# Kernel tuning notes

Measured on AMD Instinct MI355X. Metric: run time of the kernel, lower is better.

The kernel has to match this reference:

```python
import jax, jax.numpy as jnp
import numpy as np

N = 50000      # nodes
E = 800000     # edges (avg degree 16)
F_IN = 128
HID = 64
NCLS = 40
K = 2          # num_stacks
T = 2          # num_layers (shared weights)


def setup_inputs() -> dict:
    key = jax.random.key(0)
    ks = jax.random.split(key, 10)
    s = 0.05
    return {
        "x": jax.random.normal(ks[0], (N, F_IN), dtype=jnp.float32),
        "edge_index": jax.random.randint(ks[1], (2, E), 0, N),
        "w1_init": jax.random.normal(ks[2], (K, F_IN, HID), dtype=jnp.float32) * s,
        "w1": jax.random.normal(ks[3], (K, HID, HID), dtype=jnp.float32) * s,
        "v1": jax.random.normal(ks[4], (K, F_IN, HID), dtype=jnp.float32) * s,
        "b1": jax.random.normal(ks[5], (K, HID), dtype=jnp.float32) * s,
        "w2_init": jax.random.normal(ks[6], (K, HID, NCLS), dtype=jnp.float32) * s,
        "w2": jax.random.normal(ks[7], (K, NCLS, NCLS), dtype=jnp.float32) * s,
        "v2": jax.random.normal(ks[8], (K, HID, NCLS), dtype=jnp.float32) * s,
        "b2": jax.random.normal(ks[9], (K, NCLS), dtype=jnp.float32) * s,
    }


def _gcn_norm(src, dst, n):
    # PyG gcn_norm with add_self_loops=False: deg over destination, sym norm
    deg = jax.ops.segment_sum(jnp.ones_like(dst, dtype=jnp.float32), dst, num_segments=n)
    dinv = jnp.where(deg > 0, 1.0 / jnp.sqrt(deg), 0.0)
    return dinv[src] * dinv[dst]  # [E]


def _arma_conv(x, src, dst, norm, n, w_init, w, v, b, act):
    # x: [N, Fin]; w_init: [K, Fin, Fout]; w: [K, Fout, Fout]; v: [K, Fin, Fout]; b: [K, Fout]
    root = jnp.einsum('nf,kfg->kng', x, v)  # [K, N, Fout], dropout=0 -> identity
    out = None
    for t in range(T):
        if t == 0:
            h = jnp.einsum('nf,kfg->kng', x, w_init)
        else:
            h = jnp.einsum('knf,kfg->kng', out, w)
        # sparse neighbor aggregation: out[i] = sum_{(j->i)} norm_e * h[j]
        agg = jax.vmap(
            lambda hk: jax.ops.segment_sum(hk[src] * norm[:, None], dst, num_segments=n)
        )(h)  # [K, N, Fout]
        out = act(agg + root + b[:, None, :])
    return out.mean(axis=0)  # mean over stacks -> [N, Fout]


def reference(x, edge_index, w1_init, w1, v1, b1, w2_init, w2, v2, b2):
    src, dst = edge_index[0], edge_index[1]
    norm = _gcn_norm(src, dst, N)
    h = _arma_conv(x, src, dst, norm, N, w1_init, w1, v1, b1, jax.nn.relu)
    h = jax.nn.relu(h)  # wrapper ReLU; dropout is identity in eval
    o = _arma_conv(h, src, dst, norm, N, w2_init, w2, v2, b2, lambda z: z)
    return jax.nn.log_softmax(o, axis=1)
```

## Files before the change

kernel.cpp:

```cpp
#include <hip/hip_runtime.h>
#include <hip/hip_bf16.h>
#include <math.h>

#define N_NODES 50000
#define F_IN 128
#define HID 64
#define NCLS 40
#define K_STACKS 2
#define SCAN_TILE 1024
#define NBLK_CNT 256

typedef __attribute__((ext_vector_type(8))) short short8;
typedef __attribute__((ext_vector_type(4))) float floatx4;
typedef __attribute__((ext_vector_type(2))) float floatx2;

__device__ __forceinline__ unsigned int f32_to_bf16_bits(float f) {
    unsigned int u = __float_as_uint(f);
    return (u + 0x7fffu + ((u >> 16) & 1u)) >> 16;
}
__device__ __forceinline__ unsigned int pack_bf16x2(float a, float b) {
    return f32_to_bf16_bits(a) | (f32_to_bf16_bits(b) << 16);
}
__device__ __forceinline__ unsigned char f32_to_fp8(float v) {
    int pk = __builtin_amdgcn_cvt_pk_fp8_f32(v, v, 0, false);
    return (unsigned char)(pk & 0xff);
}


__global__ __launch_bounds__(256) void count_kernel(const int* __restrict__ dst,
                                                    int* __restrict__ counts,
                                                    int* __restrict__ tileSums, int E) {
    __shared__ int hist[256];
    __shared__ int ts[64];
    int blk = blockIdx.x, t = threadIdx.x;
    hist[t] = 0;
    if (t < 64) ts[t] = 0;
    __syncthreads();
    int chunk = (E + NBLK_CNT - 1) / NBLK_CNT;
    int s = blk * chunk, e = min(E, s + chunk);
    for (int i = s + t; i < e; i += 256) atomicAdd(&hist[dst[i] >> 8], 1);
    __syncthreads();
    counts[t * NBLK_CNT + blk] = hist[t];
    atomicAdd(&ts[t >> 2], hist[t]);
    __syncthreads();
    if (t < 64) atomicAdd(&tileSums[t], ts[t]);
}

__global__ __launch_bounds__(256) void scan_phase3_excl(const int* __restrict__ in,
                                                        const int* __restrict__ tileSums,
                                                        int* __restrict__ out, int n) {
    __shared__ int lds[256];
    __shared__ int tsum[64];
    int b = blockIdx.x, t = threadIdx.x;
    if (t < 64) tsum[t] = tileSums[t];
    int base = b * SCAN_TILE + t * 4;
    int e[4];
    int s = 0;
#pragma unroll
    for (int i = 0; i < 4; ++i) {
        e[i] = (base + i < n) ? in[base + i] : 0;
        s += e[i];
    }
    lds[t] = s;
    __syncthreads();
    int v = s;
    for (int off = 1; off < 256; off <<= 1) {
        int add = (t >= off) ? lds[t - off] : 0;
        __syncthreads();
        v += add;
        lds[t] = v;
        __syncthreads();
    }
    int toff = 0;
    for (int i = 0; i < b; ++i) toff += tsum[i];
    int run = (t == 0 ? 0 : lds[t - 1]) + toff;
#pragma unroll
    for (int i = 0; i < 4; ++i) {
        if (base + i < n) {
            out[base + i] = run;
            run += e[i];
        }
    }
}

__global__ __launch_bounds__(256) void bucket_scatter_kernel(const int* __restrict__ src,
                                                             const int* __restrict__ dst,
                                                             const int* __restrict__ scanned,
                                                             unsigned int* __restrict__ pairs,
                                                             int E) {
    __shared__ int cur[256];
    int blk = blockIdx.x, t = threadIdx.x;
    cur[t] = scanned[t * NBLK_CNT + blk];
    __syncthreads();
    int chunk = (E + NBLK_CNT - 1) / NBLK_CNT;
    int s0 = blk * chunk, e0 = min(E, s0 + chunk);
    for (int i = s0 + t; i < e0; i += 256) {
        int d = dst[i];
        int pos = atomicAdd(&cur[d >> 8], 1);
        pairs[pos] = (unsigned int)src[i] | ((unsigned int)(d & 255) << 16);
    }
}

__global__ __launch_bounds__(256) void csr_build_kernel(const unsigned int* __restrict__ pairs,
                                                        const int* __restrict__ scanned,
                                                        int* __restrict__ row_ptr,
                                                        float* __restrict__ dinv,
                                                        int* __restrict__ col, int N, int E) {
    __shared__ int degl[256], lds[256], curl[256], sb[2];
    int b = blockIdx.x, t = threadIdx.x;
    if (t == 0) {
        sb[0] = scanned[b * NBLK_CNT];
        sb[1] = (b + 1 < 256) ? scanned[(b + 1) * NBLK_CNT] : E;
    }
    degl[t] = 0;
    __syncthreads();
    int bstart = sb[0], bend = sb[1];
    for (int e = bstart + t; e < bend; e += 256) {
        atomicAdd(&degl[(pairs[e] >> 16) & 255], 1);
    }
    __syncthreads();
    int d = degl[t];
    lds[t] = d;
    __syncthreads();
    int v = d;
    for (int off = 1; off < 256; off <<= 1) {
        int add = (t >= off) ? lds[t - off] : 0;
        __syncthreads();
        v += add;
        lds[t] = v;
        __syncthreads();
    }
    int excl = v - d;
    int node = b * 256 + t;
    if (node <= N) row_ptr[node] = bstart + excl;
    if (node < N) dinv[node] = (d > 0) ? (1.0f / sqrtf((float)d)) : 0.0f;
    curl[t] = excl;
    __syncthreads();
    for (int e = bstart + t; e < bend; e += 256) {
        unsigned int p = pairs[e];
        int ln = (p >> 16) & 255;
        int pos = atomicAdd(&curl[ln], 1);
        col[bstart + pos] = (int)(p & 0xffffu);
    }
}

__device__ __forceinline__ void wt_one(const float* __restrict__ in,
                                       unsigned short* __restrict__ out, int li, int C, int F,
                                       int CP) {
    int k = li / (F * CP);
    int r = li - k * F * CP;
    int f = r / CP;
    int c = r - f * CP;
    out[li] = (c < C) ? (unsigned short)f32_to_bf16_bits(in[((size_t)k * C + c) * F + f]) : 0;
}

__global__ void wt_all_kernel(const float* v1, const float* w1i, const float* w1,
                              const float* v2, const float* w2i, const float* w2,
                              unsigned short* v1t, unsigned short* w1it, unsigned short* w1t,
                              unsigned short* v2t, unsigned short* w2it, unsigned short* w2t) {
    int i = blockIdx.x * blockDim.x + threadIdx.x;
    if (i < 16384) wt_one(v1, v1t, i, 128, 64, 128);
    else if (i < 32768) wt_one(w1i, w1it, i - 16384, 128, 64, 128);
    else if (i < 40960) wt_one(w1, w1t, i - 32768, 64, 64, 64);
    else if (i < 46080) wt_one(v2, v2t, i - 40960, 64, 40, 64);
    else if (i < 51200) wt_one(w2i, w2it, i - 46080, 64, 40, 64);
    else if (i < 56320) wt_one(w2, w2t, i - 51200, 40, 40, 64);
}

template <int CINP>
__device__ __forceinline__ void stage_A(const void* A, unsigned short* At, size_t abase,
                                        int n0, int t, int N, int CREAL, int a_bf16) {
    constexpr int CP8 = CINP / 8;
    constexpr int MS = CP8 - 1;
    constexpr int SH = (CP8 == 16) ? 4 : 3;
    for (int i = t; i < 64 * CP8; i += 256) {
        int n = i >> SH;
        int c = i & MS;
        uint4 w = make_uint4(0u, 0u, 0u, 0u);
        int gn = n0 + n;
        if (gn < N && c * 8 < CREAL) {
            if (a_bf16) {
                w = *(const uint4*)((const unsigned short*)A + abase + (size_t)gn * CREAL + c * 8);
            } else {
                const float* srcp = (const float*)A + abase + (size_t)gn * CREAL + c * 8;
                float4 f0 = *(const float4*)(srcp);
                float4 f1 = *(const float4*)(srcp + 4);
                w.x = pack_bf16x2(f0.x, f0.y);
                w.y = pack_bf16x2(f0.z, f0.w);
                w.z = pack_bf16x2(f1.x, f1.y);
                w.w = pack_bf16x2(f1.z, f1.w);
            }
        }
        *(uint4*)(At + n * CINP + ((c ^ (n & MS)) << 3)) = w;
    }
}

template <int CINP>
__device__ __forceinline__ void stage_B(const unsigned short* Bk, unsigned short* Bs, int t,
                                        int COUT) {
    constexpr int CP8 = CINP / 8;
    constexpr int MS = CP8 - 1;
    constexpr int SH = (CP8 == 16) ? 4 : 3;
    for (int i = t; i < COUT * CP8; i += 256) {
        int f = i >> SH;
        int c = i & MS;
        uint4 w = *(const uint4*)(Bk + f * CINP + c * 8);
        *(uint4*)(Bs + f * CINP + ((c ^ (f & MS)) << 3)) = w;
    }
}

template <int CINP>
__global__ __launch_bounds__(256) void gemm_mfma(
    const void* __restrict__ A, const unsigned short* __restrict__ Bt,
    void* __restrict__ out, const float* __restrict__ scale, int N, int COUT, int CREAL,
    int a_per_k, int a_bf16, int out_fp8, int do_scale, int out_inter) {
    constexpr int MS = CINP / 8 - 1;
    __shared__ __align__(16) unsigned short At[64 * CINP];
    __shared__ __align__(16) unsigned short Bs[64 * CINP];

    const int k = blockIdx.y;
    const int n0 = blockIdx.x * 64;
    const int t = threadIdx.x;
    stage_A<CINP>(A, At, a_per_k ? (size_t)k * N * CREAL : (size_t)0, n0, t, N, CREAL, a_bf16);
    stage_B<CINP>(Bt + (size_t)k * COUT * CINP, Bs, t, COUT);
    __syncthreads();

    const int lane = t & 63;
    const int wv = t >> 6;
    const int quad = lane >> 4;
    const int li = lane & 15;
    const int m0 = wv * 16;

    floatx4 acc[4] = {{0.f, 0.f, 0.f, 0.f}, {0.f, 0.f, 0.f, 0.f},
                      {0.f, 0.f, 0.f, 0.f}, {0.f, 0.f, 0.f, 0.f}};
    const int am = (m0 + li) & MS;
#pragma unroll
    for (int kc = 0; kc < CINP / 32; ++kc) {
        int cc = kc * 4 + quad;
        short8 a = *(const short8*)(At + (m0 + li) * CINP + ((cc ^ am) << 3));
#pragma unroll
        for (int nt = 0; nt < 4; ++nt) {
            if (nt * 16 < COUT) {
                int f = nt * 16 + li;
                short8 b = *(const short8*)(Bs + f * CINP + ((cc ^ (f & MS)) << 3));
                acc[nt] = __builtin_amdgcn_mfma_f32_16x16x32_bf16(a, b, acc[nt], 0, 0, 0);
            }
        }
    }

    float sc[4] = {1.f, 1.f, 1.f, 1.f};
    if (do_scale) {
#pragma unroll
        for (int r = 0; r < 4; ++r) {
            int node = n0 + m0 + quad * 4 + r;
            sc[r] = (node < N) ? scale[node] : 1.f;
        }
    }
#pragma unroll
    for (int nt = 0; nt < 4; ++nt) {
        if (nt * 16 >= COUT) continue;
        int f = nt * 16 + li;
        if (f >= COUT) continue;
#pragma unroll
        for (int r = 0; r < 4; ++r) {
            int node = n0 + m0 + quad * 4 + r;
            if (node < N) {
                float val = acc[nt][r] * sc[r];
                if (out_inter) {
                    size_t o = (size_t)node * 2 * COUT + (size_t)k * COUT + f;
                    if (out_fp8)
                        ((unsigned char*)out)[o] = f32_to_fp8(val);
                    else
                        ((unsigned short*)out)[o] = (unsigned short)f32_to_bf16_bits(val);
                } else {
                    size_t o = ((size_t)k * N + node) * COUT + f;
                    ((float*)out)[o] = val;
                }
            }
        }
    }
}

template <int CINP>
__global__ __launch_bounds__(256) void gemm2_mfma(
    const void* __restrict__ A, const unsigned short* __restrict__ Bt1,
    const unsigned short* __restrict__ Bt2, unsigned short* __restrict__ out1,
    unsigned char* __restrict__ out2, const float* __restrict__ scale, int N, int COUT,
    int CREAL, int a_bf16) {
    constexpr int MS = CINP / 8 - 1;
    __shared__ __align__(16) unsigned short At[64 * CINP];
    __shared__ __align__(16) unsigned short Bs1[64 * CINP];
    __shared__ __align__(16) unsigned short Bs2[64 * CINP];

    const int n0 = blockIdx.x * 64;
    const int t = threadIdx.x;
    stage_A<CINP>(A, At, (size_t)0, n0, t, N, CREAL, a_bf16);

    const int lane = t & 63;
    const int wv = t >> 6;
    const int quad = lane >> 4;
    const int li = lane & 15;
    const int m0 = wv * 16;
    const int am = (m0 + li) & MS;

    float sc[4];
#pragma unroll
    for (int r = 0; r < 4; ++r) {
        int node = n0 + m0 + quad * 4 + r;
        sc[r] = (node < N) ? scale[node] : 1.f;
    }

    for (int k = 0; k < 2; ++k) {
        if (k) __syncthreads();
        stage_B<CINP>(Bt1 + (size_t)k * COUT * CINP, Bs1, t, COUT);
        stage_B<CINP>(Bt2 + (size_t)k * COUT * CINP, Bs2, t, COUT);
        __syncthreads();

        floatx4 acc1[4] = {{0.f, 0.f, 0.f, 0.f}, {0.f, 0.f, 0.f, 0.f},
                           {0.f, 0.f, 0.f, 0.f}, {0.f, 0.f, 0.f, 0.f}};
        floatx4 acc2[4] = {{0.f, 0.f, 0.f, 0.f}, {0.f, 0.f, 0.f, 0.f},
                           {0.f, 0.f, 0.f, 0.f}, {0.f, 0.f, 0.f, 0.f}};
#pragma unroll
        for (int kc = 0; kc < CINP / 32; ++kc) {
            int cc = kc * 4 + quad;
            short8 a = *(const short8*)(At + (m0 + li) * CINP + ((cc ^ am) << 3));
#pragma unroll
            for (int nt = 0; nt < 4; ++nt) {
                if (nt * 16 < COUT) {
                    int f = nt * 16 + li;
                    int bo = f * CINP + ((cc ^ (f & MS)) << 3);
                    short8 b1 = *(const short8*)(Bs1 + bo);
                    short8 b2 = *(const short8*)(Bs2 + bo);
                    acc1[nt] = __builtin_amdgcn_mfma_f32_16x16x32_bf16(a, b1, acc1[nt], 0, 0, 0);
                    acc2[nt] = __builtin_amdgcn_mfma_f32_16x16x32_bf16(a, b2, acc2[nt], 0, 0, 0);
                }
            }
        }
#pragma unroll
        for (int nt = 0; nt < 4; ++nt) {
            if (nt * 16 >= COUT) continue;
            int f = nt * 16 + li;
            if (f >= COUT) continue;
#pragma unroll
            for (int r = 0; r < 4; ++r) {
                int node = n0 + m0 + quad * 4 + r;
                if (node < N) {
                    out1[((size_t)k * N + node) * COUT + f] =
                        (unsigned short)f32_to_bf16_bits(acc1[nt][r]);
                    out2[(size_t)node * 2 * COUT + (size_t)k * COUT + f] =
                        f32_to_fp8(acc2[nt][r] * sc[r]);
                }
            }
        }
    }
}

template <int F>
__global__ __launch_bounds__(256) void agg_kernel(
    const unsigned char* __restrict__ h8, const int* __restrict__ row_ptr,
    const int* __restrict__ col, const float* __restrict__ dinv,
    const unsigned short* __restrict__ rootb, const float* __restrict__ bias,
    void* __restrict__ out, int N, int do_relu, int mode) {
    constexpr int FH = F / 8;
    constexpr int ROWB = 2 * F;
    int wid = (blockIdx.x * blockDim.x + threadIdx.x) >> 6;
    int lane = threadIdx.x & 63;
    int half = lane >> 5;
    int l32 = lane & 31;
    int node = wid * 2 + half;
    bool valid = node < N;
    int e0 = 0, deg = 0;
    float dv = 0.f;
    if (valid) {
        e0 = row_ptr[node];
        deg = row_ptr[node + 1] - e0;
        dv = dinv[node];
    }
    const int sub = l32 >> 4;
    const int fq = l32 & 15;
    const int kk = fq >> 3;
    const int fqq = fq & 7;
    const int fqc = (fqq < FH) ? fqq : (FH - 1);
    const int foff = kk * F + fqc * 8;

    float acc[8] = {};
    for (int w0 = 0; w0 < deg; w0 += 32) {
        int mye = w0 + l32;
        int c = (mye < deg) ? col[e0 + mye] : 0;
        int nch = min(deg - w0, 32);
        for (int base = 0; base < nch; base += 16) {
            uint2 v[8];
            float wj[8];
#pragma unroll
            for (int u = 0; u < 8; ++u) {
                int j = base + u * 2 + sub;
                int cj = __shfl(c, (half << 5) | (j & 31));
                bool ok = (j < nch);
                wj[u] = ok ? 1.f : 0.f;
                int cs = ok ? cj : 0;
                v[u] = *(const uint2*)(h8 + (size_t)cs * ROWB + foff);
            }
#pragma unroll
            for (int u = 0; u < 8; ++u) {
                floatx2 f0 = __builtin_amdgcn_cvt_pk_f32_fp8(v[u].x, false);
                floatx2 f1 = __builtin_amdgcn_cvt_pk_f32_fp8(v[u].x, true);
                floatx2 f2 = __builtin_amdgcn_cvt_pk_f32_fp8(v[u].y, false);
                floatx2 f3 = __builtin_amdgcn_cvt_pk_f32_fp8(v[u].y, true);
                acc[0] += wj[u] * f0.x;
                acc[1] += wj[u] * f0.y;
                acc[2] += wj[u] * f1.x;
                acc[3] += wj[u] * f1.y;
                acc[4] += wj[u] * f2.x;
                acc[5] += wj[u] * f2.y;
                acc[6] += wj[u] * f3.x;
                acc[7] += wj[u] * f3.y;
            }
        }
    }
#pragma unroll
    for (int i = 0; i < 8; ++i) acc[i] += __shfl_xor(acc[i], 16);

    size_t oc = ((size_t)kk * N + (valid ? node : 0)) * F + fqc * 8;
    uint4 rv = *(const uint4*)(rootb + oc);
    const float* bp = bias + kk * F + fqc * 8;
    float4 b0 = *(const float4*)(bp);
    float4 b1 = *(const float4*)(bp + 4);
    const unsigned int ru[4] = {rv.x, rv.y, rv.z, rv.w};
    float res[8];
#pragma unroll
    for (int q = 0; q < 4; ++q) {
        float rlo = __uint_as_float(ru[q] << 16);
        float rhi = __uint_as_float(ru[q] & 0xffff0000u);
        float blo = (q < 2) ? ((q == 0) ? b0.x : b0.z) : ((q == 2) ? b1.x : b1.z);
        float bhi = (q < 2) ? ((q == 0) ? b0.y : b0.w) : ((q == 2) ? b1.y : b1.w);
        res[2 * q] = acc[2 * q] * dv + rlo + blo;
        res[2 * q + 1] = acc[2 * q + 1] * dv + rhi + bhi;
    }
    if (do_relu) {
#pragma unroll
        for (int i = 0; i < 8; ++i) res[i] = fmaxf(res[i], 0.f);
    }
    if (mode == 0) {
        if (sub == 0 && fqq < FH && valid) {
            size_t o = ((size_t)kk * N + node) * F + fqq * 8;
            uint4 w;
            w.x = pack_bf16x2(res[0], res[1]);
            w.y = pack_bf16x2(res[2], res[3]);
            w.z = pack_bf16x2(res[4], res[5]);
            w.w = pack_bf16x2(res[6], res[7]);
            *(uint4*)((unsigned short*)out + o) = w;
        }
    } else {
        float mres[8];
#pragma unroll
        for (int i = 0; i < 8; ++i) mres[i] = 0.5f * (res[i] + __shfl_xor(res[i], 8));
        if (mode == 1) {
            if (sub == 0 && kk == 0 && fqq < FH && valid) {
                size_t o = (size_t)node * F + fqq * 8;
                *(float4*)((float*)out + o) = make_float4(mres[0], mres[1], mres[2], mres[3]);
                *(float4*)((float*)out + o + 4) = make_float4(mres[4], mres[5], mres[6], mres[7]);
            }
        } else {
            bool act = (fqq < FH);
            float lm = -INFINITY;
            if (act) {
#pragma unroll
                for (int i = 0; i < 8; ++i) lm = fmaxf(lm, mres[i]);
            }
#pragma unroll
            for (int m = 1; m < 8; m <<= 1) lm = fmaxf(lm, __shfl_xor(lm, m));
            float ls = 0.f;
            if (act) {
#pragma unroll
                for (int i = 0; i < 8; ++i) ls += expf(mres[i] - lm);
            }
#pragma unroll
            for (int m = 1; m < 8; m <<= 1) ls += __shfl_xor(ls, m);
            float lg = lm + logf(ls);
            if (sub == 0 && kk == 0 && act && valid) {
                size_t o = (size_t)node * F + fqq * 8;
                *(float4*)((float*)out + o) =
                    make_float4(mres[0] - lg, mres[1] - lg, mres[2] - lg, mres[3] - lg);
                *(float4*)((float*)out + o + 4) =
                    make_float4(mres[4] - lg, mres[5] - lg, mres[6] - lg, mres[7] - lg);
            }
        }
    }
}


static inline size_t align256(size_t x) { return (x + 255) & ~(size_t)255; }

extern "C" void kernel_launch(void* const* d_in, const int* in_sizes, int n_in,
                              void* d_out, int out_size, void* d_ws, size_t ws_size,
                              hipStream_t stream) {
    const float* x = (const float*)d_in[0];
    const int* ei = (const int*)d_in[1];
    const float* w1_init = (const float*)d_in[2];
    const float* w1 = (const float*)d_in[3];
    const float* v1 = (const float*)d_in[4];
    const float* b1 = (const float*)d_in[5];
    const float* w2_init = (const float*)d_in[6];
    const float* w2 = (const float*)d_in[7];
    const float* v2 = (const float*)d_in[8];
    const float* b2 = (const float*)d_in[9];

    const int N = in_sizes[0] / F_IN;
    const int E = in_sizes[1] / 2;
    const int* src = ei;
    const int* dst = ei + E;

    char* p = (char*)d_ws;
    auto take = [&](size_t bytes) {
        char* r = p;
        p += align256(bytes);
        return r;
    };
    float* dinv = (float*)take((size_t)N * 4);
    int* row_ptr = (int*)take((size_t)(N + 1) * 4);
    int* tileSums = (int*)take(256 * 4);
    int* counts = (int*)take((size_t)256 * NBLK_CNT * 4);
    int* scanned = (int*)take((size_t)256 * NBLK_CNT * 4);
    unsigned int* pairs = (unsigned int*)take((size_t)E * 4);
    int* col = (int*)take((size_t)E * 4);
    unsigned short* v1t = (unsigned short*)take((size_t)2 * 64 * 128 * 2);
    unsigned short* w1it = (unsigned short*)take((size_t)2 * 64 * 128 * 2);
    unsigned short* w1t = (unsigned short*)take((size_t)2 * 64 * 64 * 2);
    unsigned short* v2t = (unsigned short*)take((size_t)2 * 40 * 64 * 2);
    unsigned short* w2it = (unsigned short*)take((size_t)2 * 40 * 64 * 2);
    unsigned short* w2t = (unsigned short*)take((size_t)2 * 40 * 64 * 2);
    unsigned short* rootb = (unsigned short*)take((size_t)K_STACKS * N * HID * 2);
    unsigned char* hb8 = (unsigned char*)take((size_t)K_STACKS * N * HID);
    unsigned short* hc = (unsigned short*)take((size_t)K_STACKS * N * HID * 2);
    float* h1 = (float*)take((size_t)N * HID * 4);

    const int TB = 256;
    const int nCnt = 256 * NBLK_CNT;
    const int nScanBlocks = nCnt / SCAN_TILE;
    const int nBuckets = (N + 255) / 256;
    const int ntiles = (N + 63) / 64;

    hipMemsetAsync(tileSums, 0, 256, stream);
    count_kernel<<<NBLK_CNT, 256, 0, stream>>>(dst, counts, tileSums, E);
    scan_phase3_excl<<<nScanBlocks, 256, 0, stream>>>(counts, tileSums, scanned, nCnt);
    bucket_scatter_kernel<<<NBLK_CNT, 256, 0, stream>>>(src, dst, scanned, pairs, E);
    csr_build_kernel<<<nBuckets, 256, 0, stream>>>(pairs, scanned, row_ptr, dinv, col, N, E);

    wt_all_kernel<<<(56320 + TB - 1) / TB, TB, 0, stream>>>(v1, w1_init, w1, v2, w2_init, w2,
                                                            v1t, w1it, w1t, v2t, w2it, w2t);

    dim3 ggrid(ntiles, K_STACKS);
    const int agg_blocks = ((N + 1) / 2 + 3) / 4;

    gemm2_mfma<128><<<ntiles, 256, 0, stream>>>(x, v1t, w1it, rootb, hb8, dinv, N, HID, 128, 0);
    agg_kernel<HID><<<agg_blocks, 256, 0, stream>>>(hb8, row_ptr, col, dinv, rootb, b1, hc, N, 1, 0);
    gemm_mfma<64><<<ggrid, 256, 0, stream>>>(hc, w1t, hb8, dinv, N, HID, 64, 1, 1, 1, 1, 1);
    agg_kernel<HID><<<agg_blocks, 256, 0, stream>>>(hb8, row_ptr, col, dinv, rootb, b1, h1, N, 1, 1);

    gemm2_mfma<64><<<ntiles, 256, 0, stream>>>(h1, v2t, w2it, rootb, hb8, dinv, N, NCLS, 64, 0);
    agg_kernel<NCLS><<<agg_blocks, 256, 0, stream>>>(hb8, row_ptr, col, dinv, rootb, b2, hc, N, 0, 0);
    gemm_mfma<64><<<ggrid, 256, 0, stream>>>(hc, w2t, hb8, dinv, N, NCLS, 40, 1, 1, 1, 1, 1);
    agg_kernel<NCLS><<<agg_blocks, 256, 0, stream>>>(hb8, row_ptr, col, dinv, rootb, b2,
                                                     (float*)d_out, N, 0, 2);
}
```

Measured before the change: 288.0 us.

## Fuse aggregation with next-layer GEMM and merge weight prep into count kernel

Fuses the first sparse aggregation of each ARMA layer with the following per-stack GEMM in a single kernel. Aggregated rows go through LDS as bf16 and are fed straight into MFMA, so the intermediate bf16 buffer is never written to or read back from global memory. It also splits gemm2 across stacks via a remapped grid, folds weight transposition into the count kernel, and has the scan compute prefix offsets directly instead of using tileSums and a memset. In exchange the fused kernel has 64 nodes per block with serialized gathers, which may lower occupancy and parallelism in the aggregation phase.

```diff
diff --git a/kernel.cpp b/kernel.cpp
--- a/kernel.cpp
+++ b/kernel.cpp
@@ -9,6 +9,7 @@
 #define K_STACKS 2
 #define SCAN_TILE 1024
 #define NBLK_CNT 256
+#define WT_BLOCKS 220
 
 typedef __attribute__((ext_vector_type(8))) short short8;
 typedef __attribute__((ext_vector_type(4))) float floatx4;
@@ -26,33 +27,55 @@
     return (unsigned char)(pk & 0xff);
 }
 
-
-__global__ __launch_bounds__(256) void count_kernel(const int* __restrict__ dst,
-                                                    int* __restrict__ counts,
-                                                    int* __restrict__ tileSums, int E) {
+__device__ __forceinline__ void wt_one(const float* __restrict__ in,
+                                       unsigned short* __restrict__ out, int li, int C, int F,
+                                       int CP) {
+    int k = li / (F * CP);
+    int r = li - k * F * CP;
+    int f = r / CP;
+    int c = r - f * CP;
+    out[li] = (c < C) ? (unsigned short)f32_to_bf16_bits(in[((size_t)k * C + c) * F + f]) : 0;
+}
+
+__global__ __launch_bounds__(256) void count_wt_kernel(
+    const int* __restrict__ dst, int* __restrict__ counts, int E,
+    const float* v1, const float* w1i, const float* w1,
+    const float* v2, const float* w2i, const float* w2,
+    unsigned short* v1t, unsigned short* w1it, unsigned short* w1t,
+    unsigned short* v2t, unsigned short* w2it, unsigned short* w2t) {
+    int blk = blockIdx.x, t = threadIdx.x;
+    if (blk >= NBLK_CNT) {
+        int i = (blk - NBLK_CNT) * 256 + t;
+        if (i < 16384) wt_one(v1, v1t, i, 128, 64, 128);
+        else if (i < 32768) wt_one(w1i, w1it, i - 16384, 128, 64, 128);
+        else if (i < 40960) wt_one(w1, w1t, i - 32768, 64, 64, 64);
+        else if (i < 46080) wt_one(v2, v2t, i - 40960, 64, 40, 64);
+        else if (i < 51200) wt_one(w2i, w2it, i - 46080, 64, 40, 64);
+        else if (i < 56320) wt_one(w2, w2t, i - 51200, 40, 40, 64);
+        return;
+    }
     __shared__ int hist[256];
-    __shared__ int ts[64];
-    int blk = blockIdx.x, t = threadIdx.x;
     hist[t] = 0;
-    if (t < 64) ts[t] = 0;
     __syncthreads();
     int chunk = (E + NBLK_CNT - 1) / NBLK_CNT;
     int s = blk * chunk, e = min(E, s + chunk);
     for (int i = s + t; i < e; i += 256) atomicAdd(&hist[dst[i] >> 8], 1);
     __syncthreads();
     counts[t * NBLK_CNT + blk] = hist[t];
-    atomicAdd(&ts[t >> 2], hist[t]);
-    __syncthreads();
-    if (t < 64) atomicAdd(&tileSums[t], ts[t]);
 }
 
 __global__ __launch_bounds__(256) void scan_phase3_excl(const int* __restrict__ in,
-                                                        const int* __restrict__ tileSums,
                                                         int* __restrict__ out, int n) {
+    __shared__ int red[256];
     __shared__ int lds[256];
-    __shared__ int tsum[64];
     int b = blockIdx.x, t = threadIdx.x;
-    if (t < 64) tsum[t] = tileSums[t];
+    int part = 0;
+    int lim = b * SCAN_TILE;
+    for (int i = t * 4; i < lim; i += 1024) {
+        int4 v = *(const int4*)(in + i);
+        part += v.x + v.y + v.z + v.w;
+    }
+    red[t] = part;
     int base = b * SCAN_TILE + t * 4;
     int e[4];
     int s = 0;
@@ -63,6 +86,11 @@
     }
     lds[t] = s;
     __syncthreads();
+    for (int off = 128; off; off >>= 1) {
+        if (t < off) red[t] += red[t + off];
+        __syncthreads();
+    }
+    int toff = red[0];
     int v = s;
     for (int off = 1; off < 256; off <<= 1) {
         int add = (t >= off) ? lds[t - off] : 0;
@@ -71,8 +99,6 @@
         lds[t] = v;
         __syncthreads();
     }
-    int toff = 0;
-    for (int i = 0; i < b; ++i) toff += tsum[i];
     int run = (t == 0 ? 0 : lds[t - 1]) + toff;
 #pragma unroll
     for (int i = 0; i < 4; ++i) {
@@ -142,29 +168,6 @@
         int pos = atomicAdd(&curl[ln], 1);
         col[bstart + pos] = (int)(p & 0xffffu);
     }
-}
-
-__device__ __forceinline__ void wt_one(const float* __restrict__ in,
-                                       unsigned short* __restrict__ out, int li, int C, int F,
-                                       int CP) {
-    int k = li / (F * CP);
-    int r = li - k * F * CP;
-    int f = r / CP;
-    int c = r - f * CP;
-    out[li] = (c < C) ? (unsigned short)f32_to_bf16_bits(in[((size_t)k * C + c) * F + f]) : 0;
-}
-
-__global__ void wt_all_kernel(const float* v1, const float* w1i, const float* w1,
-                              const float* v2, const float* w2i, const float* w2,
-                              unsigned short* v1t, unsigned short* w1it, unsigned short* w1t,
-                              unsigned short* v2t, unsigned short* w2it, unsigned short* w2t) {
-    int i = blockIdx.x * blockDim.x + threadIdx.x;
-    if (i < 16384) wt_one(v1, v1t, i, 128, 64, 128);
-    else if (i < 32768) wt_one(w1i, w1it, i - 16384, 128, 64, 128);
-    else if (i < 40960) wt_one(w1, w1t, i - 32768, 64, 64, 64);
-    else if (i < 46080) wt_one(v2, v2t, i - 40960, 64, 40, 64);
-    else if (i < 51200) wt_one(w2i, w2it, i - 46080, 64, 40, 64);
-    else if (i < 56320) wt_one(w2, w2t, i - 51200, 40, 40, 64);
 }
 
 template <int CINP>
@@ -210,78 +213,6 @@
 }
 
 template <int CINP>
-__global__ __launch_bounds__(256) void gemm_mfma(
-    const void* __restrict__ A, const unsigned short* __restrict__ Bt,
-    void* __restrict__ out, const float* __restrict__ scale, int N, int COUT, int CREAL,
-    int a_per_k, int a_bf16, int out_fp8, int do_scale, int out_inter) {
-    constexpr int MS = CINP / 8 - 1;
-    __shared__ __align__(16) unsigned short At[64 * CINP];
-    __shared__ __align__(16) unsigned short Bs[64 * CINP];
-
-    const int k = blockIdx.y;
-    const int n0 = blockIdx.x * 64;
-    const int t = threadIdx.x;
-    stage_A<CINP>(A, At, a_per_k ? (size_t)k * N * CREAL : (size_t)0, n0, t, N, CREAL, a_bf16);
-    stage_B<CINP>(Bt + (size_t)k * COUT * CINP, Bs, t, COUT);
-    __syncthreads();
-
-    const int lane = t & 63;
-    const int wv = t >> 6;
-    const int quad = lane >> 4;
-    const int li = lane & 15;
-    const int m0 = wv * 16;
-
-    floatx4 acc[4] = {{0.f, 0.f, 0.f, 0.f}, {0.f, 0.f, 0.f, 0.f},
-                      {0.f, 0.f, 0.f, 0.f}, {0.f, 0.f, 0.f, 0.f}};
-    const int am = (m0 + li) & MS;
-#pragma unroll
-    for (int kc = 0; kc < CINP / 32; ++kc) {
-        int cc = kc * 4 + quad;
-        short8 a = *(const short8*)(At + (m0 + li) * CINP + ((cc ^ am) << 3));
-#pragma unroll
-        for (int nt = 0; nt < 4; ++nt) {
-            if (nt * 16 < COUT) {
-                int f = nt * 16 + li;
-                short8 b = *(const short8*)(Bs + f * CINP + ((cc ^ (f & MS)) << 3));
-                acc[nt] = __builtin_amdgcn_mfma_f32_16x16x32_bf16(a, b, acc[nt], 0, 0, 0);
-            }
-        }
-    }
-
-    float sc[4] = {1.f, 1.f, 1.f, 1.f};
-    if (do_scale) {
-#pragma unroll
-        for (int r = 0; r < 4; ++r) {
-            int node = n0 + m0 + quad * 4 + r;
-            sc[r] = (node < N) ? scale[node] : 1.f;
-        }
-    }
-#pragma unroll
-    for (int nt = 0; nt < 4; ++nt) {
-        if (nt * 16 >= COUT) continue;
-        int f = nt * 16 + li;
-        if (f >= COUT) continue;
-#pragma unroll
-        for (int r = 0; r < 4; ++r) {
-            int node = n0 + m0 + quad * 4 + r;
-            if (node < N) {
-                float val = acc[nt][r] * sc[r];
-                if (out_inter) {
-                    size_t o = (size_t)node * 2 * COUT + (size_t)k * COUT + f;
-                    if (out_fp8)
-                        ((unsigned char*)out)[o] = f32_to_fp8(val);
-                    else
-                        ((unsigned short*)out)[o] = (unsigned short)f32_to_bf16_bits(val);
-                } else {
-                    size_t o = ((size_t)k * N + node) * COUT + f;
-                    ((float*)out)[o] = val;
-                }
-            }
-        }
-    }
-}
-
-template <int CINP>
 __global__ __launch_bounds__(256) void gemm2_mfma(
     const void* __restrict__ A, const unsigned short* __restrict__ Bt1,
     const unsigned short* __restrict__ Bt2, unsigned short* __restrict__ out1,
@@ -292,16 +223,45 @@
     __shared__ __align__(16) unsigned short Bs1[64 * CINP];
     __shared__ __align__(16) unsigned short Bs2[64 * CINP];
 
-    const int n0 = blockIdx.x * 64;
+    const int id = blockIdx.x;
+    const int p = ((id >> 4) << 3) | (id & 7);
+    const int k = (id >> 3) & 1;
+    const int ntiles = (N + 63) >> 6;
+    if (p >= ntiles) return;
+    const int n0 = p * 64;
     const int t = threadIdx.x;
     stage_A<CINP>(A, At, (size_t)0, n0, t, N, CREAL, a_bf16);
+    stage_B<CINP>(Bt1 + (size_t)k * COUT * CINP, Bs1, t, COUT);
+    stage_B<CINP>(Bt2 + (size_t)k * COUT * CINP, Bs2, t, COUT);
+    __syncthreads();
 
     const int lane = t & 63;
     const int wv = t >> 6;
     const int quad = lane >> 4;
     const int li = lane & 15;
     const int m0 = wv * 16;
+
+    floatx4 acc1[4] = {{0.f, 0.f, 0.f, 0.f}, {0.f, 0.f, 0.f, 0.f},
+                       {0.f, 0.f, 0.f, 0.f}, {0.f, 0.f, 0.f, 0.f}};
+    floatx4 acc2[4] = {{0.f, 0.f, 0.f, 0.f}, {0.f, 0.f, 0.f, 0.f},
+                       {0.f, 0.f, 0.f, 0.f}, {0.f, 0.f, 0.f, 0.f}};
     const int am = (m0 + li) & MS;
+#pragma unroll
+    for (int kc = 0; kc < CINP / 32; ++kc) {
+        int cc = kc * 4 + quad;
+        short8 a = *(const short8*)(At + (m0 + li) * CINP + ((cc ^ am) << 3));
+#pragma unroll
+        for (int nt = 0; nt < 4; ++nt) {
+            if (nt * 16 < COUT) {
+                int f = nt * 16 + li;
+                int bo = f * CINP + ((cc ^ (f & MS)) << 3);
+                short8 b1 = *(const short8*)(Bs1 + bo);
+                short8 b2 = *(const short8*)(Bs2 + bo);
+                acc1[nt] = __builtin_amdgcn_mfma_f32_16x16x32_bf16(a, b1, acc1[nt], 0, 0, 0);
+                acc2[nt] = __builtin_amdgcn_mfma_f32_16x16x32_bf16(a, b2, acc2[nt], 0, 0, 0);
+            }
+        }
+    }
 
     float sc[4];
 #pragma unroll
@@ -309,30 +269,160 @@
         int node = n0 + m0 + quad * 4 + r;
         sc[r] = (node < N) ? scale[node] : 1.f;
     }
-
+#pragma unroll
+    for (int nt = 0; nt < 4; ++nt) {
+        if (nt * 16 >= COUT) continue;
+        int f = nt * 16 + li;
+        if (f >= COUT) continue;
+#pragma unroll
+        for (int r = 0; r < 4; ++r) {
+            int node = n0 + m0 + quad * 4 + r;
+            if (node < N) {
+                out1[((size_t)k * N + node) * COUT + f] =
+                    (unsigned short)f32_to_bf16_bits(acc1[nt][r]);
+                out2[(size_t)node * 2 * COUT + (size_t)k * COUT + f] =
+                    f32_to_fp8(acc2[nt][r] * sc[r]);
+            }
+        }
+    }
+}
+
+template <int F, int CINP>
+__global__ __launch_bounds__(256) void agg_gemm_kernel(
+    const unsigned char* __restrict__ h8, const int* __restrict__ row_ptr,
+    const int* __restrict__ col, const float* __restrict__ dinv,
+    const unsigned short* __restrict__ rootb, const float* __restrict__ bias,
+    const unsigned short* __restrict__ Bt, unsigned char* __restrict__ out2,
+    int N, int do_relu) {
+    constexpr int FH = F / 8;
+    constexpr int ROWB = 2 * F;
+    constexpr int COUT = F;
+    constexpr int MS = CINP / 8 - 1;
+    __shared__ __align__(16) unsigned short At[2][64 * CINP];
+    __shared__ __align__(16) unsigned short Bs[2][64 * CINP];
+
+    const int n0 = blockIdx.x * 64;
+    const int t = threadIdx.x;
+
+    for (int i = t; i < 2 * 64 * (CINP / 8); i += 256)
+        ((uint4*)At)[i] = make_uint4(0u, 0u, 0u, 0u);
+    stage_B<CINP>(Bt, Bs[0], t, COUT);
+    stage_B<CINP>(Bt + (size_t)COUT * CINP, Bs[1], t, COUT);
+    __syncthreads();
+
+    const int lane = t & 63;
+    const int wv = t >> 6;
+    const int half = lane >> 5;
+    const int l32 = lane & 31;
+    const int sub = l32 >> 4;
+    const int fq = l32 & 15;
+    const int kk = fq >> 3;
+    const int fqq = fq & 7;
+    const int fqc = (fqq < FH) ? fqq : (FH - 1);
+    const int foff = kk * F + fqc * 8;
+
+    for (int r = 0; r < 8; ++r) {
+        int ln = r * 8 + wv * 2 + half;
+        int node = n0 + ln;
+        bool valid = node < N;
+        int e0 = 0, deg = 0;
+        float dv = 0.f;
+        if (valid) {
+            e0 = row_ptr[node];
+            deg = row_ptr[node + 1] - e0;
+            dv = dinv[node];
+        }
+        float acc[8] = {};
+        for (int w0 = 0; w0 < deg; w0 += 32) {
+            int mye = w0 + l32;
+            int c = (mye < deg) ? col[e0 + mye] : 0;
+            int nch = min(deg - w0, 32);
+            for (int base = 0; base < nch; base += 16) {
+                uint2 v[8];
+                float wj[8];
+#pragma unroll
+                for (int u = 0; u < 8; ++u) {
+                    int j = base + u * 2 + sub;
+                    int cj = __shfl(c, (half << 5) | (j & 31));
+                    bool ok = (j < nch);
+                    wj[u] = ok ? 1.f : 0.f;
+                    int cs = ok ? cj : 0;
+                    v[u] = *(const uint2*)(h8 + (size_t)cs * ROWB + foff);
+                }
+#pragma unroll
+                for (int u = 0; u < 8; ++u) {
+                    floatx2 f0 = __builtin_amdgcn_cvt_pk_f32_fp8(v[u].x, false);
+                    floatx2 f1 = __builtin_amdgcn_cvt_pk_f32_fp8(v[u].x, true);
+                    floatx2 f2 = __builtin_amdgcn_cvt_pk_f32_fp8(v[u].y, false);
+                    floatx2 f3 = __builtin_amdgcn_cvt_pk_f32_fp8(v[u].y, true);
+                    acc[0] += wj[u] * f0.x;
+                    acc[1] += wj[u] * f0.y;
+                    acc[2] += wj[u] * f1.x;
+                    acc[3] += wj[u] * f1.y;
+                    acc[4] += wj[u] * f2.x;
+                    acc[5] += wj[u] * f2.y;
+                    acc[6] += wj[u] * f3.x;
+                    acc[7] += wj[u] * f3.y;
+                }
+            }
+        }
+#pragma unroll
+        for (int i = 0; i < 8; ++i) acc[i] += __shfl_xor(acc[i], 16);
+
+        size_t oc = ((size_t)kk * N + (valid ? node : 0)) * F + fqc * 8;
+        uint4 rv = *(const uint4*)(rootb + oc);
+        const float* bp = bias + kk * F + fqc * 8;
+        float4 b0 = *(const float4*)(bp);
+        float4 b1 = *(const float4*)(bp + 4);
+        const unsigned int ru[4] = {rv.x, rv.y, rv.z, rv.w};
+        float res[8];
+#pragma unroll
+        for (int q = 0; q < 4; ++q) {
+            float rlo = __uint_as_float(ru[q] << 16);
+            float rhi = __uint_as_float(ru[q] & 0xffff0000u);
+            float blo = (q < 2) ? ((q == 0) ? b0.x : b0.z) : ((q == 2) ? b1.x : b1.z);
+            float bhi = (q < 2) ? ((q == 0) ? b0.y : b0.w) : ((q == 2) ? b1.y : b1.w);
+            res[2 * q] = acc[2 * q] * dv + rlo + blo;
+            res[2 * q + 1] = acc[2 * q + 1] * dv + rhi + bhi;
+        }
+        if (do_relu) {
+#pragma unroll
+            for (int i = 0; i < 8; ++i) res[i] = fmaxf(res[i], 0.f);
+        }
+        if (sub == 0 && fqq < FH && valid) {
+            uint4 w;
+            w.x = pack_bf16x2(res[0], res[1]);
+            w.y = pack_bf16x2(res[2], res[3]);
+            w.z = pack_bf16x2(res[4], res[5]);
+            w.w = pack_bf16x2(res[6], res[7]);
+            *(uint4*)(&At[kk][ln * CINP + ((fqq ^ (ln & MS)) << 3)]) = w;
+        }
+    }
+    __syncthreads();
+
+    const int quad = lane >> 4;
+    const int li = lane & 15;
+    const int m0 = wv * 16;
+    const int am = (m0 + li) & MS;
+    float sc[4];
+#pragma unroll
+    for (int r = 0; r < 4; ++r) {
+        int node = n0 + m0 + quad * 4 + r;
+        sc[r] = (node < N) ? dinv[node] : 1.f;
+    }
     for (int k = 0; k < 2; ++k) {
-        if (k) __syncthreads();
-        stage_B<CINP>(Bt1 + (size_t)k * COUT * CINP, Bs1, t, COUT);
-        stage_B<CINP>(Bt2 + (size_t)k * COUT * CINP, Bs2, t, COUT);
-        __syncthreads();
-
-        floatx4 acc1[4] = {{0.f, 0.f, 0.f, 0.f}, {0.f, 0.f, 0.f, 0.f},
-                           {0.f, 0.f, 0.f, 0.f}, {0.f, 0.f, 0.f, 0.f}};
-        floatx4 acc2[4] = {{0.f, 0.f, 0.f, 0.f}, {0.f, 0.f, 0.f, 0.f},
-                           {0.f, 0.f, 0.f, 0.f}, {0.f, 0.f, 0.f, 0.f}};
+        floatx4 acc[4] = {{0.f, 0.f, 0.f, 0.f}, {0.f, 0.f, 0.f, 0.f},
+                          {0.f, 0.f, 0.f, 0.f}, {0.f, 0.f, 0.f, 0.f}};
 #pragma unroll
         for (int kc = 0; kc < CINP / 32; ++kc) {
             int cc = kc * 4 + quad;
-            short8 a = *(const short8*)(At + (m0 + li) * CINP + ((cc ^ am) << 3));
+            short8 a = *(const short8*)(&At[k][(m0 + li) * CINP + ((cc ^ am) << 3)]);
 #pragma unroll
             for (int nt = 0; nt < 4; ++nt) {
                 if (nt * 16 < COUT) {
                     int f = nt * 16 + li;
-                    int bo = f * CINP + ((cc ^ (f & MS)) << 3);
-                    short8 b1 = *(const short8*)(Bs1 + bo);
-                    short8 b2 = *(const short8*)(Bs2 + bo);
-                    acc1[nt] = __builtin_amdgcn_mfma_f32_16x16x32_bf16(a, b1, acc1[nt], 0, 0, 0);
-                    acc2[nt] = __builtin_amdgcn_mfma_f32_16x16x32_bf16(a, b2, acc2[nt], 0, 0, 0);
+                    short8 b = *(const short8*)(&Bs[k][f * CINP + ((cc ^ (f & MS)) << 3)]);
+                    acc[nt] = __builtin_amdgcn_mfma_f32_16x16x32_bf16(a, b, acc[nt], 0, 0, 0);
                 }
             }
         }
@@ -344,12 +434,9 @@
 #pragma unroll
             for (int r = 0; r < 4; ++r) {
                 int node = n0 + m0 + quad * 4 + r;
-                if (node < N) {
-                    out1[((size_t)k * N + node) * COUT + f] =
-                        (unsigned short)f32_to_bf16_bits(acc1[nt][r]);
+                if (node < N)
                     out2[(size_t)node * 2 * COUT + (size_t)k * COUT + f] =
-                        f32_to_fp8(acc2[nt][r] * sc[r]);
-                }
+                        f32_to_fp8(acc[nt][r] * sc[r]);
             }
         }
     }
@@ -440,50 +527,38 @@
 #pragma unroll
         for (int i = 0; i < 8; ++i) res[i] = fmaxf(res[i], 0.f);
     }
-    if (mode == 0) {
-        if (sub == 0 && fqq < FH && valid) {
-            size_t o = ((size_t)kk * N + node) * F + fqq * 8;
-            uint4 w;
-            w.x = pack_bf16x2(res[0], res[1]);
-            w.y = pack_bf16x2(res[2], res[3]);
-            w.z = pack_bf16x2(res[4], res[5]);
-            w.w = pack_bf16x2(res[6], res[7]);
-            *(uint4*)((unsigned short*)out + o) = w;
+    float mres[8];
+#pragma unroll
+    for (int i = 0; i < 8; ++i) mres[i] = 0.5f * (res[i] + __shfl_xor(res[i], 8));
+    if (mode == 1) {
+        if (sub == 0 && kk == 0 && fqq < FH && valid) {
+            size_t o = (size_t)node * F + fqq * 8;
+            *(float4*)((float*)out + o) = make_float4(mres[0], mres[1], mres[2], mres[3]);
+            *(float4*)((float*)out + o + 4) = make_float4(mres[4], mres[5], mres[6], mres[7]);
         }
     } else {
-        float mres[8];
-#pragma unroll
-        for (int i = 0; i < 8; ++i) mres[i] = 0.5f * (res[i] + __shfl_xor(res[i], 8));
-        if (mode == 1) {
-            if (sub == 0 && kk == 0 && fqq < FH && valid) {
-                size_t o = (size_t)node * F + fqq * 8;
-                *(float4*)((float*)out + o) = make_float4(mres[0], mres[1], mres[2], mres[3]);
-                *(float4*)((float*)out + o + 4) = make_float4(mres[4], mres[5], mres[6], mres[7]);
-            }
-        } else {
-            bool act = (fqq < FH);
-            float lm = -INFINITY;
-            if (act) {
-#pragma unroll
-                for (int i = 0; i < 8; ++i) lm = fmaxf(lm, mres[i]);
-            }
-#pragma unroll
-            for (int m = 1; m < 8; m <<= 1) lm = fmaxf(lm, __shfl_xor(lm, m));
-            float ls = 0.f;
-            if (act) {
-#pragma unroll
-                for (int i = 0; i < 8; ++i) ls += expf(mres[i] - lm);
-            }
-#pragma unroll
-            for (int m = 1; m < 8; m <<= 1) ls += __shfl_xor(ls, m);
-            float lg = lm + logf(ls);
-            if (sub == 0 && kk == 0 && act && valid) {
-                size_t o = (size_t)node * F + fqq * 8;
-                *(float4*)((float*)out + o) =
-                    make_float4(mres[0] - lg, mres[1] - lg, mres[2] - lg, mres[3] - lg);
-                *(float4*)((float*)out + o + 4) =
-                    make_float4(mres[4] - lg, mres[5] - lg, mres[6] - lg, mres[7] - lg);
-            }
+        bool act = (fqq < FH);
+        float lm = -INFINITY;
+        if (act) {
+#pragma unroll
+            for (int i = 0; i < 8; ++i) lm = fmaxf(lm, mres[i]);
+        }
+#pragma unroll
+        for (int m = 1; m < 8; m <<= 1) lm = fmaxf(lm, __shfl_xor(lm, m));
+        float ls = 0.f;
+        if (act) {
+#pragma unroll
+            for (int i = 0; i < 8; ++i) ls += expf(mres[i] - lm);
+        }
+#pragma unroll
+        for (int m = 1; m < 8; m <<= 1) ls += __shfl_xor(ls, m);
+        float lg = lm + logf(ls);
+        if (sub == 0 && kk == 0 && act && valid) {
+            size_t o = (size_t)node * F + fqq * 8;
+            *(float4*)((float*)out + o) =
+                make_float4(mres[0] - lg, mres[1] - lg, mres[2] - lg, mres[3] - lg);
+            *(float4*)((float*)out + o + 4) =
+                make_float4(mres[4] - lg, mres[5] - lg, mres[6] - lg, mres[7] - lg);
         }
     }
 }
@@ -518,7 +593,6 @@
     };
     float* dinv = (float*)take((size_t)N * 4);
     int* row_ptr = (int*)take((size_t)(N + 1) * 4);
-    int* tileSums = (int*)take(256 * 4);
     int* counts = (int*)take((size_t)256 * NBLK_CNT * 4);
     int* scanned = (int*)take((size_t)256 * NBLK_CNT * 4);
     unsigned int* pairs = (unsigned int*)take((size_t)E * 4);
@@ -531,35 +605,31 @@
     unsigned short* w2t = (unsigned short*)take((size_t)2 * 40 * 64 * 2);
     unsigned short* rootb = (unsigned short*)take((size_t)K_STACKS * N * HID * 2);
     unsigned char* hb8 = (unsigned char*)take((size_t)K_STACKS * N * HID);
-    unsigned short* hc = (unsigned short*)take((size_t)K_STACKS * N * HID * 2);
+    unsigned char* hb8b = (unsigned char*)take((size_t)K_STACKS * N * HID);
     float* h1 = (float*)take((size_t)N * HID * 4);
 
-    const int TB = 256;
     const int nCnt = 256 * NBLK_CNT;
     const int nScanBlocks = nCnt / SCAN_TILE;
     const int nBuckets = (N + 255) / 256;
     const int ntiles = (N + 63) / 64;
-
-    hipMemsetAsync(tileSums, 0, 256, stream);
-    count_kernel<<<NBLK_CNT, 256, 0, stream>>>(dst, counts, tileSums, E);
-    scan_phase3_excl<<<nScanBlocks, 256, 0, stream>>>(counts, tileSums, scanned, nCnt);
+    const int g2grid = ((ntiles + 7) / 8) * 16;
+    const int agg_blocks = ((N + 1) / 2 + 3) / 4;
+
+    count_wt_kernel<<<NBLK_CNT + WT_BLOCKS, 256, 0, stream>>>(
+        dst, counts, E, v1, w1_init, w1, v2, w2_init, w2, v1t, w1it, w1t, v2t, w2it, w2t);
+    scan_phase3_excl<<<nScanBlocks, 256, 0, stream>>>(counts, scanned, nCnt);
     bucket_scatter_kernel<<<NBLK_CNT, 256, 0, stream>>>(src, dst, scanned, pairs, E);
     csr_build_kernel<<<nBuckets, 256, 0, stream>>>(pairs, scanned, row_ptr, dinv, col, N, E);
 
-    wt_all_kernel<<<(56320 + TB - 1) / TB, TB, 0, stream>>>(v1, w1_init, w1, v2, w2_init, w2,
-                                                            v1t, w1it, w1t, v2t, w2it, w2t);
-
-    dim3 ggrid(ntiles, K_STACKS);
-    const int agg_blocks = ((N + 1) / 2 + 3) / 4;
-
-    gemm2_mfma<128><<<ntiles, 256, 0, stream>>>(x, v1t, w1it, rootb, hb8, dinv, N, HID, 128, 0);
-    agg_kernel<HID><<<agg_blocks, 256, 0, stream>>>(hb8, row_ptr, col, dinv, rootb, b1, hc, N, 1, 0);
-    gemm_mfma<64><<<ggrid, 256, 0, stream>>>(hc, w1t, hb8, dinv, N, HID, 64, 1, 1, 1, 1, 1);
-    agg_kernel<HID><<<agg_blocks, 256, 0, stream>>>(hb8, row_ptr, col, dinv, rootb, b1, h1, N, 1, 1);
-
-    gemm2_mfma<64><<<ntiles, 256, 0, stream>>>(h1, v2t, w2it, rootb, hb8, dinv, N, NCLS, 64, 0);
-    agg_kernel<NCLS><<<agg_blocks, 256, 0, stream>>>(hb8, row_ptr, col, dinv, rootb, b2, hc, N, 0, 0);
-    gemm_mfma<64><<<ggrid, 256, 0, stream>>>(hc, w2t, hb8, dinv, N, NCLS, 40, 1, 1, 1, 1, 1);
-    agg_kernel<NCLS><<<agg_blocks, 256, 0, stream>>>(hb8, row_ptr, col, dinv, rootb, b2,
+    gemm2_mfma<128><<<g2grid, 256, 0, stream>>>(x, v1t, w1it, rootb, hb8, dinv, N, HID, 128, 0);
+    agg_gemm_kernel<64, 64><<<ntiles, 256, 0, stream>>>(hb8, row_ptr, col, dinv, rootb, b1,
+                                                        w1t, hb8b, N, 1);
+    agg_kernel<HID><<<agg_blocks, 256, 0, stream>>>(hb8b, row_ptr, col, dinv, rootb, b1, h1,
+                                                    N, 1, 1);
+
+    gemm2_mfma<64><<<g2grid, 256, 0, stream>>>(h1, v2t, w2it, rootb, hb8, dinv, N, NCLS, 64, 0);
+    agg_gemm_kernel<40, 64><<<ntiles, 256, 0, stream>>>(hb8, row_ptr, col, dinv, rootb, b2,
+                                                        w2t, hb8b, N, 0);
+    agg_kernel<NCLS><<<agg_blocks, 256, 0, stream>>>(hb8b, row_ptr, col, dinv, rootb, b2,
                                                      (float*)d_out, N, 0, 2);
 }
```

New measurement: 316.6 us. 1.1x slower.
